# Kernel tuning notes

Hardware: AMD Instinct MI355X
Metric: run time of the kernel (lower is better)

## Reference

```python
import jax, jax.numpy as jnp
import numpy as np

DIM = 2048
HEAD_DIM = 64
N_HEADS = 16
N_KV_HEADS = 4
RANK = 8
ALPHA = 16
LORA_SCALE = ALPHA / RANK  # 2.0
SEQ = 2048
BATCH = 1
ROPE_THETA = 10000.0


def setup_inputs() -> dict:
    key = jax.random.key(0)
    ks = jax.random.split(key, 12)
    std = 0.02
    x = jax.random.normal(ks[0], (BATCH, SEQ, DIM), dtype=jnp.float32)
    # rope tables: (SEQ, HEAD_DIM//2, 2) = (cos, sin)
    inv_freq = 1.0 / (ROPE_THETA ** (jnp.arange(0, HEAD_DIM, 2, dtype=jnp.float32) / HEAD_DIM))
    ang = jnp.arange(SEQ, dtype=jnp.float32)[:, None] * inv_freq[None, :]
    freq_cis = jnp.stack([jnp.cos(ang), jnp.sin(ang)], axis=-1)
    mk = lambda k, shp: (jax.random.normal(k, shp, dtype=jnp.float32) * std)
    return {
        "x": x,
        "freq_cis": freq_cis,
        "wq": mk(ks[1], (HEAD_DIM, DIM)),
        "wq_a": mk(ks[2], (RANK, DIM)),
        "wq_b": mk(ks[3], (N_HEADS * HEAD_DIM, RANK)),
        "wk": mk(ks[4], (HEAD_DIM, DIM)),
        "wk_a": mk(ks[5], (RANK, DIM)),
        "wk_b": mk(ks[6], (N_KV_HEADS * HEAD_DIM, RANK)),
        "wv": mk(ks[7], (HEAD_DIM, DIM)),
        "wv_a": mk(ks[8], (RANK, DIM)),
        "wv_b": mk(ks[9], (N_KV_HEADS * HEAD_DIM, RANK)),
        "wo": mk(ks[10], (DIM, HEAD_DIM)),
        "wo_share": mk(ks[11], (DIM, N_HEADS * HEAD_DIM)),
    }


def _shared_plus_lora(x, w_base, w_a, w_b, n_heads):
    # base: single head (B,S,HEAD_DIM) broadcast across heads; LoRA adds per-head delta
    base = jnp.einsum('bsd,hd->bsh', x, w_base)                    # (B,S,Dh)
    delta = jnp.einsum('bsr,or->bso', jnp.einsum('bsd,rd->bsr', x, w_a), w_b) * LORA_SCALE
    B, S, _ = x.shape
    delta = delta.reshape(B, S, n_heads, HEAD_DIM)
    return base[:, :, None, :] + delta                             # (B,S,H,Dh)


def _rope(t, freq_cis):
    # t: (B,S,H,Dh); freq_cis: (S, Dh//2, 2)
    B, S, H, D = t.shape
    tr = t.reshape(B, S, H, D // 2, 2)
    cos = freq_cis[:, None, :, 0]  # (S,1,Dh//2)
    sin = freq_cis[:, None, :, 1]
    xr, xi = tr[..., 0], tr[..., 1]
    out = jnp.stack([xr * cos - xi * sin, xr * sin + xi * cos], axis=-1)
    return out.reshape(B, S, H, D)


def reference(x, freq_cis, wq, wq_a, wq_b, wk, wk_a, wk_b, wv, wv_a, wv_b, wo, wo_share):
    B, S, _ = x.shape
    g = N_HEADS // N_KV_HEADS
    xq = _shared_plus_lora(x, wq, wq_a, wq_b, N_HEADS)      # (B,S,H,Dh)
    xk = _shared_plus_lora(x, wk, wk_a, wk_b, N_KV_HEADS)   # (B,S,Hkv,Dh)
    xv = _shared_plus_lora(x, wv, wv_a, wv_b, N_KV_HEADS)
    xq = _rope(xq, freq_cis[:S])
    xk = _rope(xk, freq_cis[:S])
    # GQA attention without materializing repeat_kv: group q heads per kv head
    q = xq.reshape(B, S, N_KV_HEADS, g, HEAD_DIM)
    scale = 1.0 / jnp.sqrt(jnp.asarray(HEAD_DIM, dtype=x.dtype))
    scores = jnp.einsum('bskgd,btkd->bkgst', q, xk) * scale  # (B,Hkv,g,S,S)
    causal = jnp.tril(jnp.ones((S, S), dtype=bool))
    scores = jnp.where(causal, scores, jnp.asarray(-jnp.inf, dtype=scores.dtype))
    p = jax.nn.softmax(scores, axis=-1)
    out = jnp.einsum('bkgst,btkd->bskgd', p, xv).reshape(B, S, N_HEADS, HEAD_DIM)
    # output projection: shared base applied per-head then summed + LoRA-style shared delta
    base = jnp.einsum('bshd,ed->bse', out, wo)
    delta = jnp.einsum('bsf,ef->bse', out.reshape(B, S, N_HEADS * HEAD_DIM), wo_share)
    return base + delta
```

## Files before the change

### kernel.cpp

```cpp
#include <hip/hip_runtime.h>
#include <hip/hip_bf16.h>

#define DEV __device__ __forceinline__

typedef unsigned short u16;
typedef __attribute__((ext_vector_type(8))) short short8;
typedef __attribute__((ext_vector_type(4))) float f32x4;
typedef __attribute__((ext_vector_type(16))) float f32x16;

DEV u16 f2bf(float f) {
  union { float f; unsigned u; } v; v.f = f;
  unsigned r = v.u + 0x7FFFu + ((v.u >> 16) & 1u);
  return (u16)(r >> 16);
}

DEV unsigned cvtpk(float lo, float hi) {
  unsigned r;
  asm("v_cvt_pk_bf16_f32 %0, %1, %2" : "=v"(r) : "v"(lo), "v"(hi));
  return r;
}

DEV void async_ld16(const u16* g, u16* l) {
  __builtin_amdgcn_global_load_lds((__attribute__((address_space(1))) void*)g,
                                   (__attribute__((address_space(3))) void*)l,
                                   16, 0, 0);
}

DEV f32x4 mfma16(short8 a, short8 b, f32x4 c) {
  return __builtin_amdgcn_mfma_f32_16x16x32_bf16(a, b, c, 0, 0, 0);
}
DEV f32x16 mfma32(short8 a, short8 b, f32x16 c) {
  return __builtin_amdgcn_mfma_f32_32x32x16_bf16(a, b, c, 0, 0, 0);
}

DEV short8 mkfrag(unsigned w0, unsigned w1, unsigned w2, unsigned w3) {
  union { unsigned u[4]; short8 s; } u;
  u.u[0] = w0; u.u[1] = w1; u.u[2] = w2; u.u[3] = w3;
  return u.s;
}

DEV short8 lds_rd(const u16* buf, int row, int colb) {
  return *(const short8*)((const char*)buf + row*128 + (colb ^ ((row & 7) << 4)));
}

#define QSCALE (0.125f * 1.4426950408889634f)

__global__ __launch_bounds__(256) void k_prep(const float* __restrict__ x,
    const float* __restrict__ wq, const float* __restrict__ wk,
    const float* __restrict__ wv, const float* __restrict__ wqa,
    const float* __restrict__ wka, const float* __restrict__ wva,
    const float* __restrict__ wo, const float* __restrict__ wos,
    u16* __restrict__ xb, u16* __restrict__ W1, u16* __restrict__ Weff) {
  const int bid = blockIdx.x;
  if (bid < 1024) {
    int i = bid*256 + threadIdx.x;
    for (; i < 1048576; i += 1024*256) {
      float4 v = ((const float4*)x)[i];
      ushort4 o;
      o.x = f2bf(v.x); o.y = f2bf(v.y); o.z = f2bf(v.z); o.w = f2bf(v.w);
      ((ushort4*)xb)[i] = o;
    }
  } else if (bid < 1280) {
    const int row = bid - 1024;
    const float* src = nullptr; float sc = 1.f;
    if (row < 64)       { src = wq  + row*2048;       sc = QSCALE; }
    else if (row < 128) { src = wk  + (row-64)*2048;  }
    else if (row < 192) { src = wv  + (row-128)*2048; }
    else if (row < 200) { src = wqa + (row-192)*2048; sc = 2.f*QSCALE; }
    else if (row < 208) { src = wka + (row-200)*2048; sc = 2.f; }
    else if (row < 216) { src = wva + (row-208)*2048; sc = 2.f; }
    for (int c = threadIdx.x; c < 2048; c += 256)
      W1[row*2048 + c] = src ? f2bf(src[c]*sc) : (u16)0;
  } else {
    const int e = bid - 1280;
    for (int f = threadIdx.x; f < 1024; f += 256)
      Weff[e*1024 + f] = f2bf(wos[e*1024 + f] + wo[e*64 + (f & 63)]);
  }
}

template<int BM, int BN>
__global__ __launch_bounds__(512)
void k_gemm_bt(const u16* __restrict__ A, const u16* __restrict__ B,
               float* __restrict__ C, int M, int N, int K, int kslice) {
  constexpr int NWC = (BN >= 128) ? 4 : 2;
  constexpr int NWR = 8 / NWC;
  constexpr int WM = BM / NWR, WN = BN / NWC;
  constexpr int FM = WM/16, FN = WN/16;
  __shared__ u16 As[BM*64];
  __shared__ u16 Bs[BN*64];
  const int tid = threadIdx.x;
  const int w = tid >> 6, l = tid & 63;
  const int wm = (w / NWC)*WM, wn = (w % NWC)*WN;
  const int tm = blockIdx.y*BM, tn = blockIdx.x*BN;
  const int k0 = blockIdx.z * kslice;
  C += (size_t)blockIdx.z * M * N;
  const int sr = (w << 3) + (l >> 3);
  const int sc = (((l & 7) ^ (l >> 3)) << 3);
  const int la = l & 15, lg = l >> 4;

  f32x4 acc[FM][FN];
#pragma unroll
  for (int i = 0; i < FM; ++i)
#pragma unroll
    for (int j = 0; j < FN; ++j) acc[i][j] = (f32x4){0.f,0.f,0.f,0.f};

  const int nk = kslice >> 6;
  for (int kt = 0; kt < nk; ++kt) {
    const int kk = k0 + (kt << 6);
#pragma unroll
    for (int j = 0; j < BM/64; ++j)
      async_ld16(A + (size_t)(tm + j*64 + sr)*K + kk + sc, &As[(j*64 + w*8)*64]);
#pragma unroll
    for (int j = 0; j < BN/64; ++j)
      async_ld16(B + (size_t)(tn + j*64 + sr)*K + kk + sc, &Bs[(j*64 + w*8)*64]);
    __syncthreads();
    short8 af[FM][2], bfr[FN][2];
#pragma unroll
    for (int mi = 0; mi < FM; ++mi)
#pragma unroll
      for (int ks = 0; ks < 2; ++ks)
        af[mi][ks] = lds_rd(As, wm + mi*16 + la, ks*64 + lg*16);
#pragma unroll
    for (int ni = 0; ni < FN; ++ni)
#pragma unroll
      for (int ks = 0; ks < 2; ++ks)
        bfr[ni][ks] = lds_rd(Bs, wn + ni*16 + la, ks*64 + lg*16);
#pragma unroll
    for (int ks = 0; ks < 2; ++ks)
#pragma unroll
      for (int mi = 0; mi < FM; ++mi)
#pragma unroll
        for (int ni = 0; ni < FN; ++ni)
          acc[mi][ni] = mfma16(af[mi][ks], bfr[ni][ks], acc[mi][ni]);
    __syncthreads();
  }
#pragma unroll
  for (int mi = 0; mi < FM; ++mi)
#pragma unroll
    for (int ni = 0; ni < FN; ++ni) {
      const int r0 = tm + wm + mi*16 + lg*4;
      const int cc = tn + wn + ni*16 + la;
#pragma unroll
      for (int r = 0; r < 4; ++r)
        C[(size_t)(r0 + r)*N + cc] = acc[mi][ni][r];
    }
}

__global__ __launch_bounds__(256)
void k_expand(const float* __restrict__ proj, const float* __restrict__ wqb,
              const float* __restrict__ wkb, const float* __restrict__ wvb,
              const float* __restrict__ freq, u16* __restrict__ Q,
              u16* __restrict__ Kb, u16* __restrict__ Vt) {
  __shared__ float prs[256];
  const int s = blockIdx.x;
  {
    const int c = threadIdx.x;
    const float* p0 = proj + s*256;
    prs[c] = (p0[c] + p0[c + 524288]) + (p0[c + 1048576] + p0[c + 1572864]);
  }
  __syncthreads();
  const int d = threadIdx.x & 63;
  const int w = threadIdx.x >> 6;
  const float cs = freq[s*64 + (d & 62)];
  const float sn = freq[s*64 + (d & 62) + 1];
#pragma unroll
  for (int pass = 0; pass < 6; ++pass) {
    const int slot = pass*4 + w;
    int bcol, tb; const float* wb;
    if (slot < 16)      { bcol = 0;   tb = 192; wb = wqb + (slot*64 + d)*8; }
    else if (slot < 20) { bcol = 64;  tb = 200; wb = wkb + ((slot-16)*64 + d)*8; }
    else                { bcol = 128; tb = 208; wb = wvb + ((slot-20)*64 + d)*8; }
    float val = prs[bcol + d];
#pragma unroll
    for (int r = 0; r < 8; ++r) val += prs[tb + r] * wb[r];
    if (slot < 20) {
      float partner = __shfl_xor(val, 1);
      val = (d & 1) ? (partner*sn + val*cs) : (val*cs - partner*sn);
    }
    u16 o = f2bf(val);
    if (slot < 16)      Q [((size_t)slot*2048 + s)*64 + d] = o;
    else if (slot < 20) Kb[((size_t)(slot-16)*2048 + s)*64 + d] = o;
    else                Vt[(size_t)(slot-20)*131072 + (size_t)d*2048 + s] = o;
  }
}

__global__ __launch_bounds__(256, 4)
void k_attn(const u16* __restrict__ Q, const u16* __restrict__ Kb,
            const u16* __restrict__ Vt, u16* __restrict__ O) {
  __shared__ float comb[3][64][33];
  __shared__ u16 scr[2048];
  const int w = threadIdx.x >> 6, l = threadIdx.x & 63;
  const int bid = blockIdx.x;
  const int h = bid & 15, kh = h >> 2;
  const int z = bid >> 4;
  const int a = z & 15, b = z >> 4;
  const int qs = (b << 4) | ((b & 1) ? (15 - a) : a);
  const int q0 = qs*32;
  const int lq = l & 31, hh = l >> 5;
  const int qg = q0 + lq;

  const u16* Qh = Q  + (size_t)h *131072;
  const u16* Kh = Kb + (size_t)kh*131072;
  const u16* Vh = Vt + (size_t)kh*131072;

  short8 bq[4];
#pragma unroll
  for (int ks = 0; ks < 4; ++ks)
    bq[ks] = *(const short8*)&Qh[qg*64 + ks*16 + hh*8];

  f32x16 acc0, acc1;
#pragma unroll
  for (int r = 0; r < 16; ++r) { acc0[r] = 0.f; acc1[r] = 0.f; }
  float lsum = 0.f;
  const float SM = 20.f;

  const int nt = (qs >> 1) + 1;

  for (int tt = w; tt < nt; tt += 4) {
    const int t0 = tt*64;
    const u16* kr0 = Kh + (size_t)(t0 + lq)*64 + hh*8;
    const u16* kr1 = kr0 + 32*64;
    short8 ak0[4], ak1[4];
#pragma unroll
    for (int ks = 0; ks < 4; ++ks) {
      ak0[ks] = *(const short8*)(kr0 + ks*16);
      ak1[ks] = *(const short8*)(kr1 + ks*16);
    }
    f32x16 s0, s1;
#pragma unroll
    for (int r = 0; r < 16; ++r) { s0[r] = 0.f; s1[r] = 0.f; }
    __builtin_amdgcn_s_setprio(1);
#pragma unroll
    for (int ks = 0; ks < 4; ++ks) {
      s0 = mfma32(ak0[ks], bq[ks], s0);
      s1 = mfma32(ak1[ks], bq[ks], s1);
    }
    __builtin_amdgcn_s_setprio(0);

    const u16* vr0 = Vh + (size_t)lq*2048 + t0 + hh*8;
    const u16* vr1 = vr0 + (size_t)32*2048;
    short8 av0[4], av1[4];
#pragma unroll
    for (int kb = 0; kb < 4; ++kb) {
      av0[kb] = *(const short8*)(vr0 + kb*16);
      av1[kb] = *(const short8*)(vr1 + kb*16);
    }

    if (t0 + 63 > q0) {
#pragma unroll
      for (int r = 0; r < 16; ++r) {
        const int tl = (r & 3) + ((r >> 2) << 3) + (hh << 2);
        if (t0 + tl > qg)      s0[r] = -1e30f;
        if (t0 + 32 + tl > qg) s1[r] = -1e30f;
      }
    }

    unsigned cwa[4][2], cwb[4][2];
    float psum = 0.f;
#pragma unroll
    for (int rq = 0; rq < 4; ++rq) {
      float a0 = exp2f(s0[4*rq+0] - SM), a1 = exp2f(s0[4*rq+1] - SM);
      float a2 = exp2f(s0[4*rq+2] - SM), a3 = exp2f(s0[4*rq+3] - SM);
      float b0 = exp2f(s1[4*rq+0] - SM), b1 = exp2f(s1[4*rq+1] - SM);
      float b2 = exp2f(s1[4*rq+2] - SM), b3 = exp2f(s1[4*rq+3] - SM);
      psum += (a0+a1) + (a2+a3) + (b0+b1) + (b2+b3);
      cwa[rq][0] = cvtpk(a0, a1); cwa[rq][1] = cvtpk(a2, a3);
      cwb[rq][0] = cvtpk(b0, b1); cwb[rq][1] = cvtpk(b2, b3);
    }
    lsum += psum;
    unsigned ya0 = __shfl_xor(hh ? cwa[0][0] : cwa[1][0], 32);
    unsigned ya1 = __shfl_xor(hh ? cwa[0][1] : cwa[1][1], 32);
    unsigned ya2 = __shfl_xor(hh ? cwa[2][0] : cwa[3][0], 32);
    unsigned ya3 = __shfl_xor(hh ? cwa[2][1] : cwa[3][1], 32);
    unsigned yb0 = __shfl_xor(hh ? cwb[0][0] : cwb[1][0], 32);
    unsigned yb1 = __shfl_xor(hh ? cwb[0][1] : cwb[1][1], 32);
    unsigned yb2 = __shfl_xor(hh ? cwb[2][0] : cwb[3][0], 32);
    unsigned yb3 = __shfl_xor(hh ? cwb[2][1] : cwb[3][1], 32);
    short8 pa0 = hh ? mkfrag(ya0, ya1, cwa[1][0], cwa[1][1])
                    : mkfrag(cwa[0][0], cwa[0][1], ya0, ya1);
    short8 pa1 = hh ? mkfrag(ya2, ya3, cwa[3][0], cwa[3][1])
                    : mkfrag(cwa[2][0], cwa[2][1], ya2, ya3);
    short8 pb0 = hh ? mkfrag(yb0, yb1, cwb[1][0], cwb[1][1])
                    : mkfrag(cwb[0][0], cwb[0][1], yb0, yb1);
    short8 pb1 = hh ? mkfrag(yb2, yb3, cwb[3][0], cwb[3][1])
                    : mkfrag(cwb[2][0], cwb[2][1], yb2, yb3);

    __builtin_amdgcn_s_setprio(1);
    acc0 = mfma32(av0[0], pa0, acc0); acc1 = mfma32(av1[0], pa0, acc1);
    acc0 = mfma32(av0[1], pa1, acc0); acc1 = mfma32(av1[1], pa1, acc1);
    acc0 = mfma32(av0[2], pb0, acc0); acc1 = mfma32(av1[2], pb0, acc1);
    acc0 = mfma32(av0[3], pb1, acc0); acc1 = mfma32(av1[3], pb1, acc1);
    __builtin_amdgcn_s_setprio(0);
  }

  if (w > 0) {
    float* cb = &comb[w-1][l][0];
#pragma unroll
    for (int r = 0; r < 16; ++r) { cb[r] = acc0[r]; cb[16+r] = acc1[r]; }
    cb[32] = lsum;
  }
  __syncthreads();
  if (w == 0) {
#pragma unroll
    for (int j = 0; j < 3; ++j) {
      const float* cb = &comb[j][l][0];
#pragma unroll
      for (int r = 0; r < 16; ++r) { acc0[r] += cb[r]; acc1[r] += cb[16+r]; }
      lsum += cb[32];
    }
    lsum += __shfl_xor(lsum, 32);
    const float inv = 1.f / lsum;
#pragma unroll
    for (int dt = 0; dt < 2; ++dt)
#pragma unroll
      for (int rq = 0; rq < 4; ++rq) {
        float v0 = (dt ? acc1[4*rq+0] : acc0[4*rq+0]) * inv;
        float v1 = (dt ? acc1[4*rq+1] : acc0[4*rq+1]) * inv;
        float v2 = (dt ? acc1[4*rq+2] : acc0[4*rq+2]) * inv;
        float v3 = (dt ? acc1[4*rq+3] : acc0[4*rq+3]) * inv;
        const int dby = dt*64 + rq*16 + hh*8;
        const int by = lq*128 + (dby ^ ((lq & 7) << 4));
        *(unsigned*)((char*)scr + by)     = cvtpk(v0, v1);
        *(unsigned*)((char*)scr + by + 4) = cvtpk(v2, v3);
      }
#pragma unroll
    for (int qq = 0; qq < 4; ++qq) {
      const int qrow = qq*8 + (l >> 3);
      const int by = qrow*128 + (((l & 7) << 4) ^ ((qrow & 7) << 4));
      short8 v = *(const short8*)((const char*)scr + by);
      *(short8*)&O[(size_t)(q0 + qrow)*1024 + h*64 + (l & 7)*8] = v;
    }
  }
}

extern "C" void kernel_launch(void* const* d_in, const int* in_sizes, int n_in,
                              void* d_out, int out_size, void* d_ws, size_t ws_size,
                              hipStream_t stream) {
  const float* x    = (const float*)d_in[0];
  const float* freq = (const float*)d_in[1];
  const float* wq   = (const float*)d_in[2];
  const float* wqa  = (const float*)d_in[3];
  const float* wqb  = (const float*)d_in[4];
  const float* wk   = (const float*)d_in[5];
  const float* wka  = (const float*)d_in[6];
  const float* wkb  = (const float*)d_in[7];
  const float* wv   = (const float*)d_in[8];
  const float* wva  = (const float*)d_in[9];
  const float* wvb  = (const float*)d_in[10];
  const float* wo   = (const float*)d_in[11];
  const float* wos  = (const float*)d_in[12];
  float* out = (float*)d_out;

  char* ws = (char*)d_ws;
  u16*  x_bf = (u16*)ws;
  u16*  Qb   = (u16*)ws;
  u16*  Kbuf = (u16*)(ws + (4u<<20));
  u16*  Vtb  = (u16*)(ws + (5u<<20));
  u16*  W1   = (u16*)(ws + (8u<<20));
  u16*  Weff = (u16*)(ws + (9u<<20));
  float* proj = (float*)(ws + (13u<<20));
  u16*  Obf  = (u16*)(ws + (13u<<20));

  k_prep    <<<3328, 256, 0, stream>>>(x, wq, wk, wv, wqa, wka, wva, wo, wos,
                                       x_bf, W1, Weff);
  k_gemm_bt<128,64><<<dim3(4,16,4), 512, 0, stream>>>(x_bf, W1, proj, 2048, 256, 2048, 512);
  k_expand  <<<dim3(2048), 256, 0, stream>>>(proj, wqb, wkb, wvb, freq, Qb, Kbuf, Vtb);
  k_attn    <<<dim3(1024), 256, 0, stream>>>(Qb, Kbuf, Vtb, Obf);
  k_gemm_bt<128,128><<<dim3(16,16,1), 512, 0, stream>>>(Obf, Weff, out, 2048, 2048, 1024, 1024);
}
```

Baseline: 94.32 us.

## Stage K/V tiles through LDS asynchronously, shrink attention tiles, retune GEMM splits

The attention kernel now prefetches each wave's next 32-key K and V tile into a swizzled LDS buffer with async global-to-LDS loads, reading MFMA fragments from LDS instead of global memory. The key tile drops from 64 to 32, so there are twice as many iterations, each with half the MFMAs. The projection GEMM split-K count goes from 4 to 8, with k_expand summing 8 partials, and the output GEMM tile changes from 128x128 to 64x128. These trade more loop overhead and partial-sum traffic for latency hiding and more blocks in flight.

```diff
diff --git a/kernel.cpp b/kernel.cpp
--- a/kernel.cpp
+++ b/kernel.cpp
@@ -156,7 +156,9 @@
   {
     const int c = threadIdx.x;
     const float* p0 = proj + s*256;
-    prs[c] = (p0[c] + p0[c + 524288]) + (p0[c + 1048576] + p0[c + 1572864]);
+    float t0 = (p0[c]             + p0[c +  524288]) + (p0[c + 1048576] + p0[c + 1572864]);
+    float t1 = (p0[c + 2097152] + p0[c + 2621440]) + (p0[c + 3145728] + p0[c + 3670016]);
+    prs[c] = t0 + t1;
   }
   __syncthreads();
   const int d = threadIdx.x & 63;
@@ -187,8 +189,7 @@
 __global__ __launch_bounds__(256, 4)
 void k_attn(const u16* __restrict__ Q, const u16* __restrict__ Kb,
             const u16* __restrict__ Vt, u16* __restrict__ O) {
-  __shared__ float comb[3][64][33];
-  __shared__ u16 scr[2048];
+  __shared__ __align__(16) char smem[33792];
   const int w = threadIdx.x >> 6, l = threadIdx.x & 63;
   const int bid = blockIdx.x;
   const int h = bid & 15, kh = h >> 2;
@@ -199,6 +200,9 @@
   const int lq = l & 31, hh = l >> 5;
   const int qg = q0 + lq;
 
+  u16* kbuf = (u16*)(smem + w*8192);
+  u16* vbuf = (u16*)(smem + w*8192 + 4096);
+
   const u16* Qh = Q  + (size_t)h *131072;
   const u16* Kh = Kb + (size_t)kh*131072;
   const u16* Vh = Vt + (size_t)kh*131072;
@@ -214,87 +218,90 @@
   float lsum = 0.f;
   const float SM = 20.f;
 
-  const int nt = (qs >> 1) + 1;
+  const int nt = qs + 1;
+
+#define STAGE(T0)                                                         \
+  {                                                                       \
+    const int t0_ = (T0);                                                 \
+    _Pragma("unroll")                                                     \
+    for (int j = 0; j < 4; ++j) {                                         \
+      const int c = j*64 + l;                                             \
+      const int row = c >> 3, e = (c & 7) ^ (row & 7);                    \
+      async_ld16(Kh + (size_t)(t0_ + row)*64 + e*8, kbuf + j*512);        \
+      const int dd = row + (e >> 2)*32;                                   \
+      async_ld16(Vh + (size_t)dd*2048 + t0_ + (e & 3)*8, vbuf + j*512);   \
+    }                                                                     \
+  }
+
+  if (w < nt) STAGE(w*32);
 
   for (int tt = w; tt < nt; tt += 4) {
-    const int t0 = tt*64;
-    const u16* kr0 = Kh + (size_t)(t0 + lq)*64 + hh*8;
-    const u16* kr1 = kr0 + 32*64;
-    short8 ak0[4], ak1[4];
-#pragma unroll
-    for (int ks = 0; ks < 4; ++ks) {
-      ak0[ks] = *(const short8*)(kr0 + ks*16);
-      ak1[ks] = *(const short8*)(kr1 + ks*16);
-    }
-    f32x16 s0, s1;
-#pragma unroll
-    for (int r = 0; r < 16; ++r) { s0[r] = 0.f; s1[r] = 0.f; }
+    asm volatile("s_waitcnt vmcnt(0)" ::: "memory");
+    __builtin_amdgcn_sched_barrier(0);
+    short8 ak[4], av[2][2];
+#pragma unroll
+    for (int ks = 0; ks < 4; ++ks)
+      ak[ks] = lds_rd(kbuf, lq, ks*32 + hh*16);
+#pragma unroll
+    for (int dh = 0; dh < 2; ++dh)
+#pragma unroll
+      for (int k2 = 0; k2 < 2; ++k2)
+        av[dh][k2] = lds_rd(vbuf, lq, (dh*4 + k2*2 + hh)*16);
+    asm volatile("s_waitcnt lgkmcnt(0)" ::: "memory");
+    __builtin_amdgcn_sched_barrier(0);
+    if (tt + 4 < nt) STAGE((tt + 4)*32);
+
+    f32x16 s;
+#pragma unroll
+    for (int r = 0; r < 16; ++r) s[r] = 0.f;
     __builtin_amdgcn_s_setprio(1);
 #pragma unroll
-    for (int ks = 0; ks < 4; ++ks) {
-      s0 = mfma32(ak0[ks], bq[ks], s0);
-      s1 = mfma32(ak1[ks], bq[ks], s1);
-    }
+    for (int ks = 0; ks < 4; ++ks)
+      s = mfma32(ak[ks], bq[ks], s);
     __builtin_amdgcn_s_setprio(0);
 
-    const u16* vr0 = Vh + (size_t)lq*2048 + t0 + hh*8;
-    const u16* vr1 = vr0 + (size_t)32*2048;
-    short8 av0[4], av1[4];
-#pragma unroll
-    for (int kb = 0; kb < 4; ++kb) {
-      av0[kb] = *(const short8*)(vr0 + kb*16);
-      av1[kb] = *(const short8*)(vr1 + kb*16);
-    }
-
-    if (t0 + 63 > q0) {
+    const int t0 = tt*32;
+    if (t0 + 31 > q0) {
 #pragma unroll
       for (int r = 0; r < 16; ++r) {
         const int tl = (r & 3) + ((r >> 2) << 3) + (hh << 2);
-        if (t0 + tl > qg)      s0[r] = -1e30f;
-        if (t0 + 32 + tl > qg) s1[r] = -1e30f;
+        if (t0 + tl > qg) s[r] = -1e30f;
       }
     }
 
-    unsigned cwa[4][2], cwb[4][2];
+    unsigned cw[4][2];
     float psum = 0.f;
 #pragma unroll
     for (int rq = 0; rq < 4; ++rq) {
-      float a0 = exp2f(s0[4*rq+0] - SM), a1 = exp2f(s0[4*rq+1] - SM);
-      float a2 = exp2f(s0[4*rq+2] - SM), a3 = exp2f(s0[4*rq+3] - SM);
-      float b0 = exp2f(s1[4*rq+0] - SM), b1 = exp2f(s1[4*rq+1] - SM);
-      float b2 = exp2f(s1[4*rq+2] - SM), b3 = exp2f(s1[4*rq+3] - SM);
-      psum += (a0+a1) + (a2+a3) + (b0+b1) + (b2+b3);
-      cwa[rq][0] = cvtpk(a0, a1); cwa[rq][1] = cvtpk(a2, a3);
-      cwb[rq][0] = cvtpk(b0, b1); cwb[rq][1] = cvtpk(b2, b3);
+      float a0 = exp2f(s[4*rq+0] - SM), a1 = exp2f(s[4*rq+1] - SM);
+      float a2 = exp2f(s[4*rq+2] - SM), a3 = exp2f(s[4*rq+3] - SM);
+      psum += (a0 + a1) + (a2 + a3);
+      cw[rq][0] = cvtpk(a0, a1); cw[rq][1] = cvtpk(a2, a3);
     }
     lsum += psum;
-    unsigned ya0 = __shfl_xor(hh ? cwa[0][0] : cwa[1][0], 32);
-    unsigned ya1 = __shfl_xor(hh ? cwa[0][1] : cwa[1][1], 32);
-    unsigned ya2 = __shfl_xor(hh ? cwa[2][0] : cwa[3][0], 32);
-    unsigned ya3 = __shfl_xor(hh ? cwa[2][1] : cwa[3][1], 32);
-    unsigned yb0 = __shfl_xor(hh ? cwb[0][0] : cwb[1][0], 32);
-    unsigned yb1 = __shfl_xor(hh ? cwb[0][1] : cwb[1][1], 32);
-    unsigned yb2 = __shfl_xor(hh ? cwb[2][0] : cwb[3][0], 32);
-    unsigned yb3 = __shfl_xor(hh ? cwb[2][1] : cwb[3][1], 32);
-    short8 pa0 = hh ? mkfrag(ya0, ya1, cwa[1][0], cwa[1][1])
-                    : mkfrag(cwa[0][0], cwa[0][1], ya0, ya1);
-    short8 pa1 = hh ? mkfrag(ya2, ya3, cwa[3][0], cwa[3][1])
-                    : mkfrag(cwa[2][0], cwa[2][1], ya2, ya3);
-    short8 pb0 = hh ? mkfrag(yb0, yb1, cwb[1][0], cwb[1][1])
-                    : mkfrag(cwb[0][0], cwb[0][1], yb0, yb1);
-    short8 pb1 = hh ? mkfrag(yb2, yb3, cwb[3][0], cwb[3][1])
-                    : mkfrag(cwb[2][0], cwb[2][1], yb2, yb3);
+    unsigned y00 = __shfl_xor(hh ? cw[0][0] : cw[1][0], 32);
+    unsigned y01 = __shfl_xor(hh ? cw[0][1] : cw[1][1], 32);
+    unsigned y10 = __shfl_xor(hh ? cw[2][0] : cw[3][0], 32);
+    unsigned y11 = __shfl_xor(hh ? cw[2][1] : cw[3][1], 32);
+    short8 p0 = hh ? mkfrag(y00, y01, cw[1][0], cw[1][1])
+                   : mkfrag(cw[0][0], cw[0][1], y00, y01);
+    short8 p1 = hh ? mkfrag(y10, y11, cw[3][0], cw[3][1])
+                   : mkfrag(cw[2][0], cw[2][1], y10, y11);
 
     __builtin_amdgcn_s_setprio(1);
-    acc0 = mfma32(av0[0], pa0, acc0); acc1 = mfma32(av1[0], pa0, acc1);
-    acc0 = mfma32(av0[1], pa1, acc0); acc1 = mfma32(av1[1], pa1, acc1);
-    acc0 = mfma32(av0[2], pb0, acc0); acc1 = mfma32(av1[2], pb0, acc1);
-    acc0 = mfma32(av0[3], pb1, acc0); acc1 = mfma32(av1[3], pb1, acc1);
+    acc0 = mfma32(av[0][0], p0, acc0);
+    acc1 = mfma32(av[1][0], p0, acc1);
+    acc0 = mfma32(av[0][1], p1, acc0);
+    acc1 = mfma32(av[1][1], p1, acc1);
     __builtin_amdgcn_s_setprio(0);
   }
-
+#undef STAGE
+
+  __syncthreads();
+  float* comb = (float*)smem;
+  u16* scr = (u16*)(smem + 26624);
   if (w > 0) {
-    float* cb = &comb[w-1][l][0];
+    float* cb = comb + ((w-1)*64 + l)*33;
 #pragma unroll
     for (int r = 0; r < 16; ++r) { cb[r] = acc0[r]; cb[16+r] = acc1[r]; }
     cb[32] = lsum;
@@ -303,7 +310,7 @@
   if (w == 0) {
 #pragma unroll
     for (int j = 0; j < 3; ++j) {
-      const float* cb = &comb[j][l][0];
+      const float* cb = comb + (j*64 + l)*33;
 #pragma unroll
       for (int r = 0; r < 16; ++r) { acc0[r] += cb[r]; acc1[r] += cb[16+r]; }
       lsum += cb[32];
@@ -363,8 +370,8 @@
 
   k_prep    <<<3328, 256, 0, stream>>>(x, wq, wk, wv, wqa, wka, wva, wo, wos,
                                        x_bf, W1, Weff);
-  k_gemm_bt<128,64><<<dim3(4,16,4), 512, 0, stream>>>(x_bf, W1, proj, 2048, 256, 2048, 512);
+  k_gemm_bt<128,64><<<dim3(4,16,8), 512, 0, stream>>>(x_bf, W1, proj, 2048, 256, 2048, 256);
   k_expand  <<<dim3(2048), 256, 0, stream>>>(proj, wqb, wkb, wvb, freq, Qb, Kbuf, Vtb);
   k_attn    <<<dim3(1024), 256, 0, stream>>>(Qb, Kbuf, Vtb, Obf);
-  k_gemm_bt<128,128><<<dim3(16,16,1), 512, 0, stream>>>(Obf, Weff, out, 2048, 2048, 1024, 1024);
-}
+  k_gemm_bt<64,128><<<dim3(16,32,1), 512, 0, stream>>>(Obf, Weff, out, 2048, 2048, 1024, 1024);
+}
```

Result: faster. 87.74 us (-7.0%).
